# Optimization experiments

Measured on AMD Instinct MI355X. Metric: run time of the kernel, lower is better.

## Reference

```python
import jax, jax.numpy as jnp
import numpy as np

B, T, D, FF, H, K = 8, 1024, 512, 2048, 8, 15
HD = D // H  # key_dim = d_model // num_heads


def _ln(x, g, b):
    # keras LayerNormalization default epsilon = 1e-3
    m = jnp.mean(x, axis=-1, keepdims=True)
    v = jnp.var(x, axis=-1, keepdims=True)
    return (x - m) * jax.lax.rsqrt(v + 1e-3) * g + b


def setup_inputs() -> dict:
    key = jax.random.key(0)
    ks = iter(jax.random.split(key, 64))

    def rn(shape, s=0.02):
        return jax.random.normal(next(ks), shape, jnp.float32) * s

    p = {}
    p['x'] = jax.random.normal(next(ks), (B, T, D), jnp.float32)
    # ff_pre: LN -> Dense(FF, relu) -> Dense(D)
    p['g1'] = jnp.ones((D,), jnp.float32); p['b1'] = jnp.zeros((D,), jnp.float32)
    p['Wff1'] = rn((D, FF)); p['bff1'] = jnp.zeros((FF,), jnp.float32)
    p['Wff2'] = rn((FF, D)); p['bff2'] = jnp.zeros((D,), jnp.float32)
    # attention norm + MHA projections (keras EinsumDense shapes)
    p['ga'] = jnp.ones((D,), jnp.float32); p['ba'] = jnp.zeros((D,), jnp.float32)
    p['Wq'] = rn((D, H, HD)); p['bq'] = jnp.zeros((H, HD), jnp.float32)
    p['Wk'] = rn((D, H, HD)); p['bk'] = jnp.zeros((H, HD), jnp.float32)
    p['Wv'] = rn((D, H, HD)); p['bv'] = jnp.zeros((H, HD), jnp.float32)
    p['Wo'] = rn((H, HD, D)); p['bo'] = jnp.zeros((D,), jnp.float32)
    # conv branch: LN -> pointwise conv (2D, gelu) -> depthwise conv(k=15) -> BN -> swish -> pointwise conv (D)
    p['gc'] = jnp.ones((D,), jnp.float32); p['bc'] = jnp.zeros((D,), jnp.float32)
    p['Wcp'] = rn((D, 2 * D)); p['bcp'] = jnp.zeros((2 * D,), jnp.float32)
    p['dwk'] = rn((K, 1, 2 * D)); p['dwb'] = jnp.zeros((2 * D,), jnp.float32)
    p['bn_g'] = jnp.ones((2 * D,), jnp.float32); p['bn_b'] = jnp.zeros((2 * D,), jnp.float32)
    p['bn_m'] = jnp.zeros((2 * D,), jnp.float32)
    p['bn_v'] = jnp.ones((2 * D,), jnp.float32)
    p['Wco'] = rn((2 * D, D)); p['bco'] = jnp.zeros((D,), jnp.float32)
    # ff_post
    p['g2'] = jnp.ones((D,), jnp.float32); p['b2'] = jnp.zeros((D,), jnp.float32)
    p['Wf1'] = rn((D, FF)); p['bf1'] = jnp.zeros((FF,), jnp.float32)
    p['Wf2'] = rn((FF, D)); p['bf2'] = jnp.zeros((D,), jnp.float32)
    return p


def reference(x, g1, b1, Wff1, bff1, Wff2, bff2, ga, ba, Wq, bq, Wk, bk, Wv, bv, Wo, bo, gc, bc, Wcp, bcp, dwk, dwb, bn_g, bn_b, bn_m, bn_v, Wco, bco, g2, b2, Wf1, bf1, Wf2, bf2):
    # Macaron FFN (pre), half-step residual applied later
    x_ff = jnp.maximum(_ln(x, g1, b1) @ Wff1 + bff1, 0.0) @ Wff2 + bff2

    # causal multi-head self-attention (cache=None path)
    a = _ln(x, ga, ba)
    q = jnp.einsum('btd,dhk->bthk', a, Wq) + bq
    k = jnp.einsum('btd,dhk->bthk', a, Wk) + bk
    v = jnp.einsum('btd,dhk->bthk', a, Wv) + bv
    scores = jnp.einsum('bqhd,bkhd->bhqk', q, k) / jnp.sqrt(jnp.float32(HD))
    causal = jnp.tril(jnp.ones((T, T), bool))  # [T,T]
    scores = jnp.where(causal, scores, jnp.float32(-1e9))
    w = jax.nn.softmax(scores, axis=-1)
    ctx = jnp.einsum('bhqk,bkhd->bqhd', w, v)
    attn = jnp.einsum('bqhd,hdo->bqo', ctx, Wo) + bo

    x = x + 0.5 * x_ff + attn

    # convolution module: pointwise(gelu) -> causal left-pad -> depthwise -> BN(inference) -> swish -> pointwise
    c = jax.nn.gelu(_ln(x, gc, bc) @ Wcp + bcp, approximate=False)
    c = jnp.pad(c, ((0, 0), (K - 1, 0), (0, 0)))  # causal pad
    c = jax.lax.conv_general_dilated(
        c, dwk, window_strides=(1,), padding='VALID',
        dimension_numbers=('NWC', 'WIO', 'NWC'), feature_group_count=2 * D) + dwb
    c = (c - bn_m) * jax.lax.rsqrt(bn_v + 1e-3) * bn_g + bn_b
    c = c * jax.nn.sigmoid(c)  # swish
    c = c @ Wco + bco
    x = x + c

    # post FFN (full residual)
    x = x + (jnp.maximum(_ln(x, g2, b2) @ Wf1 + bf1, 0.0) @ Wf2 + bf2)
    return x
```

## Files before the change

kernel.cpp:

```cpp
#include <hip/hip_runtime.h>
#include <hip/hip_bf16.h>
#include <math.h>

#define BB 8
#define TT 1024
#define DD 512
#define FFD 2048
#define HH 8
#define HDD 64
#define KW 15
#define MR (BB*TT)
#define QKVN 1536

typedef __attribute__((ext_vector_type(8))) short short8;
typedef __attribute__((ext_vector_type(4))) short short4v;
typedef __attribute__((ext_vector_type(4))) float f32x4;
typedef __hip_bfloat16 bf16;

__device__ __forceinline__ float bf2f(unsigned u16) {
    return __uint_as_float(u16 << 16);
}

__device__ __forceinline__ void async_copy16(const void* g, void* l) {
    __builtin_amdgcn_global_load_lds(
        (const __attribute__((address_space(1))) void*)g,
        (__attribute__((address_space(3))) void*)l, 16, 0, 0);
}

__device__ __forceinline__ float gelu_exact(float v) {
    return 0.5f * v * (1.0f + erff(v * 0.70710678118654752f));
}

struct PrepPack {
    const float* src[10];
    bf16*        dst[10];
    int          K[10];
    int          lgNT[10];
    float        scale[10];
    int          off[10];
    const float* bq; const float* bk; const float* bv;
    float*       bdst;
    const float* x;
    const float* g1; const float* b1; const float* ga; const float* ba;
    bf16* o1; bf16* o2;
};

__global__ __launch_bounds__(256) void prep_kernel(PrepPack P) {
    __shared__ alignas(16) bf16 T[64][72];
    const int bid = blockIdx.x;
    if (bid == 1536) {
        #pragma unroll
        for (int it = 0; it < 6; ++it) {
            int i = it * 256 + threadIdx.x;
            float v = i < 512 ? P.bq[i] * 0.125f
                              : (i < 1024 ? P.bk[i - 512] : P.bv[i - 1024]);
            P.bdst[i] = v;
        }
        return;
    }
    if (bid > 1536) {
        int wave = ((bid - 1537) * 256 + (int)threadIdx.x) >> 6;
        int lane = threadIdx.x & 63;
        const float* row = P.x + (size_t)wave * DD;
        float4 v0 = ((const float4*)row)[lane];
        float4 v1 = ((const float4*)row)[64 + lane];
        float s  = v0.x + v0.y + v0.z + v0.w + v1.x + v1.y + v1.z + v1.w;
        float ss = v0.x*v0.x + v0.y*v0.y + v0.z*v0.z + v0.w*v0.w
                 + v1.x*v1.x + v1.y*v1.y + v1.z*v1.z + v1.w*v1.w;
        #pragma unroll
        for (int off = 32; off >= 1; off >>= 1) {
            s  += __shfl_xor(s,  off, 64);
            ss += __shfl_xor(ss, off, 64);
        }
        float mean = s * (1.0f / DD);
        float var  = ss * (1.0f / DD) - mean * mean;
        float r    = rsqrtf(var + 1e-3f);
        float n0x = (v0.x - mean) * r, n0y = (v0.y - mean) * r,
              n0z = (v0.z - mean) * r, n0w = (v0.w - mean) * r;
        float n1x = (v1.x - mean) * r, n1y = (v1.y - mean) * r,
              n1z = (v1.z - mean) * r, n1w = (v1.w - mean) * r;
        {
            float4 g0 = ((const float4*)P.g1)[lane];
            float4 gg = ((const float4*)P.g1)[64 + lane];
            float4 b0 = ((const float4*)P.b1)[lane];
            float4 bb = ((const float4*)P.b1)[64 + lane];
            alignas(8) bf16 o0[4], o1[4];
            o0[0] = __float2bfloat16(n0x * g0.x + b0.x);
            o0[1] = __float2bfloat16(n0y * g0.y + b0.y);
            o0[2] = __float2bfloat16(n0z * g0.z + b0.z);
            o0[3] = __float2bfloat16(n0w * g0.w + b0.w);
            o1[0] = __float2bfloat16(n1x * gg.x + bb.x);
            o1[1] = __float2bfloat16(n1y * gg.y + bb.y);
            o1[2] = __float2bfloat16(n1z * gg.z + bb.z);
            o1[3] = __float2bfloat16(n1w * gg.w + bb.w);
            bf16* orow = P.o1 + (size_t)wave * DD;
            *(short4v*)(orow + lane * 4)       = *(const short4v*)o0;
            *(short4v*)(orow + 256 + lane * 4) = *(const short4v*)o1;
        }
        {
            float4 g0 = ((const float4*)P.ga)[lane];
            float4 gg = ((const float4*)P.ga)[64 + lane];
            float4 b0 = ((const float4*)P.ba)[lane];
            float4 bb = ((const float4*)P.ba)[64 + lane];
            alignas(8) bf16 o0[4], o1[4];
            o0[0] = __float2bfloat16(n0x * g0.x + b0.x);
            o0[1] = __float2bfloat16(n0y * g0.y + b0.y);
            o0[2] = __float2bfloat16(n0z * g0.z + b0.z);
            o0[3] = __float2bfloat16(n0w * g0.w + b0.w);
            o1[0] = __float2bfloat16(n1x * gg.x + bb.x);
            o1[1] = __float2bfloat16(n1y * gg.y + bb.y);
            o1[2] = __float2bfloat16(n1z * gg.z + bb.z);
            o1[3] = __float2bfloat16(n1w * gg.w + bb.w);
            bf16* orow = P.o2 + (size_t)wave * DD;
            *(short4v*)(orow + lane * 4)       = *(const short4v*)o0;
            *(short4v*)(orow + 256 + lane * 4) = *(const short4v*)o1;
        }
        return;
    }
    int e = 0;
    #pragma unroll
    for (int i = 1; i < 10; ++i) e = (bid >= P.off[i]) ? i : e;
    const float* W  = P.src[e];
    bf16*        Wt = P.dst[e];
    const int    K  = P.K[e];
    const int    lg = P.lgNT[e];
    const float  scale = P.scale[e];
    const int local = bid - P.off[e];
    const int bx = local & ((1 << lg) - 1);
    const int by = local >> lg;
    const int k0 = by * 64;
    const int n0 = bx * 64;
    const int N  = (1 << lg) * 64;
    const int tid = threadIdx.x;
    #pragma unroll
    for (int it = 0; it < 4; ++it) {
        int lin = it * 256 + tid;
        int kl  = lin >> 4;
        int nq  = (lin & 15) * 4;
        float4 v = *(const float4*)(W + (size_t)(k0 + kl) * N + n0 + nq);
        T[nq + 0][kl] = __float2bfloat16(v.x * scale);
        T[nq + 1][kl] = __float2bfloat16(v.y * scale);
        T[nq + 2][kl] = __float2bfloat16(v.z * scale);
        T[nq + 3][kl] = __float2bfloat16(v.w * scale);
    }
    __syncthreads();
    #pragma unroll
    for (int it = 0; it < 4; ++it) {
        int lin = it * 256 + tid;
        int nl  = lin >> 4;
        int kq  = (lin & 15) * 4;
        *(short4v*)(Wt + (size_t)(n0 + nl) * K + k0 + kq) = *(const short4v*)&T[nl][kq];
    }
}

__global__ __launch_bounds__(256) void ln_kernel(const float* __restrict__ x,
                                                 const float* __restrict__ g,
                                                 const float* __restrict__ b,
                                                 bf16* __restrict__ out) {
    int wave = (blockIdx.x * blockDim.x + threadIdx.x) >> 6;
    int lane = threadIdx.x & 63;
    if (wave >= MR) return;
    const float* row = x + (size_t)wave * DD;
    float4 v0 = ((const float4*)row)[lane];
    float4 v1 = ((const float4*)row)[64 + lane];
    float s  = v0.x + v0.y + v0.z + v0.w + v1.x + v1.y + v1.z + v1.w;
    float ss = v0.x*v0.x + v0.y*v0.y + v0.z*v0.z + v0.w*v0.w
             + v1.x*v1.x + v1.y*v1.y + v1.z*v1.z + v1.w*v1.w;
    #pragma unroll
    for (int off = 32; off >= 1; off >>= 1) {
        s  += __shfl_xor(s,  off, 64);
        ss += __shfl_xor(ss, off, 64);
    }
    float mean = s * (1.0f / DD);
    float var  = ss * (1.0f / DD) - mean * mean;
    float r    = rsqrtf(var + 1e-3f);
    float4 g0 = ((const float4*)g)[lane];
    float4 g1 = ((const float4*)g)[64 + lane];
    float4 b0 = ((const float4*)b)[lane];
    float4 b1 = ((const float4*)b)[64 + lane];
    alignas(8) bf16 o0[4], o1[4];
    o0[0] = __float2bfloat16((v0.x - mean) * r * g0.x + b0.x);
    o0[1] = __float2bfloat16((v0.y - mean) * r * g0.y + b0.y);
    o0[2] = __float2bfloat16((v0.z - mean) * r * g0.z + b0.z);
    o0[3] = __float2bfloat16((v0.w - mean) * r * g0.w + b0.w);
    o1[0] = __float2bfloat16((v1.x - mean) * r * g1.x + b1.x);
    o1[1] = __float2bfloat16((v1.y - mean) * r * g1.y + b1.y);
    o1[2] = __float2bfloat16((v1.z - mean) * r * g1.z + b1.z);
    o1[3] = __float2bfloat16((v1.w - mean) * r * g1.w + b1.w);
    bf16* orow = out + (size_t)wave * DD;
    *(short4v*)(orow + lane * 4)       = *(const short4v*)o0;
    *(short4v*)(orow + 256 + lane * 4) = *(const short4v*)o1;
}

template<int BN, int OP, int RESMODE, int OUTMODE>
__global__ __launch_bounds__(256) void bgemm_kernel(
    const bf16* __restrict__ A,
    const bf16* __restrict__ Bt,
    const float* __restrict__ bias,
    const float* __restrict__ res1,
    const bf16* __restrict__ res2,
    float s2, float oscale,
    void* __restrict__ Cout,
    int N, int Kd, int nxb)
{
    constexpr int NT = BN / 32;
    __shared__ alignas(16) bf16 As[128][64];
    __shared__ alignas(16) bf16 Bs[BN][64];
    const int tid  = threadIdx.x;
    const int w    = tid >> 6;
    const int lane = tid & 63;
    const int quad = lane >> 4;
    const int l16  = lane & 15;
    const int wm   = w >> 1, wn = w & 1;

    const int flat = blockIdx.x;
    const int c8   = flat & 7;
    const int j    = flat >> 3;
    const int jy   = j / nxb;
    const int m0   = (c8 * 8 + jy) * 128;
    const int n0   = (j - jy * nxb) * BN;

    const int srow = lane >> 3;
    const int scol = ((lane & 7) ^ srow) * 8;

    const bf16* Ap = A  + (size_t)(m0 + w * 32 + srow) * Kd + scol;
    const bf16* Bp = Bt + (size_t)(n0 + w * (BN / 4) + srow) * Kd + scol;

    f32x4 acc[4][NT] = {};

    for (int k0 = 0; k0 < Kd; k0 += 64) {
        #pragma unroll
        for (int i = 0; i < 4; ++i)
            async_copy16(Ap + (size_t)(i * 8) * Kd + k0, &As[w * 32 + i * 8][0]);
        #pragma unroll
        for (int i = 0; i < BN / 32; ++i)
            async_copy16(Bp + (size_t)(i * 8) * Kd + k0, &Bs[w * (BN / 4) + i * 8][0]);
        __syncthreads();
        #pragma unroll
        for (int ks = 0; ks < 2; ++ks) {
            short8 af[4], bfr[NT];
            #pragma unroll
            for (int mt = 0; mt < 4; ++mt) {
                const int row = wm * 64 + mt * 16 + l16;
                const int c   = ((ks * 4 + quad) ^ (row & 7)) * 16;
                af[mt] = *(const short8*)((const char*)&As[row][0] + c);
            }
            #pragma unroll
            for (int nt = 0; nt < NT; ++nt) {
                const int col = wn * (BN / 2) + nt * 16 + l16;
                const int c   = ((ks * 4 + quad) ^ (col & 7)) * 16;
                bfr[nt] = *(const short8*)((const char*)&Bs[col][0] + c);
            }
            #pragma unroll
            for (int mt = 0; mt < 4; ++mt)
                #pragma unroll
                for (int nt = 0; nt < NT; ++nt)
                    acc[mt][nt] = __builtin_amdgcn_mfma_f32_16x16x32_bf16(
                        af[mt], bfr[nt], acc[mt][nt], 0, 0, 0);
        }
        __syncthreads();
    }

    const int crow0 = m0 + wm * 64 + quad * 4;
    const int ccol0 = n0 + wn * (BN / 2) + l16;
    #pragma unroll
    for (int nt = 0; nt < NT; ++nt) {
        const int col = ccol0 + nt * 16;
        const float bv = bias[col];
        #pragma unroll
        for (int mt = 0; mt < 4; ++mt) {
            #pragma unroll
            for (int r = 0; r < 4; ++r) {
                const int row = crow0 + mt * 16 + r;
                const size_t off = (size_t)row * N + col;
                float o = acc[mt][nt][r] + bv;
                if (OP == 1)      o = fmaxf(o, 0.f);
                else if (OP == 2) o = gelu_exact(o);
                if (RESMODE >= 1) o += res1[off];
                if (RESMODE == 2) o += s2 * __bfloat162float(res2[off]);
                if (OUTMODE == 0) ((float*)Cout)[off] = o;
                else              ((bf16*)Cout)[off]  = __float2bfloat16(o * oscale);
            }
        }
    }
}

__global__ __launch_bounds__(256) void ffqkv_kernel(
    const bf16* __restrict__ lnb, const bf16* __restrict__ lnab,
    const bf16* __restrict__ Wff1t, const bf16* __restrict__ Wqkvt,
    const float* __restrict__ bff1, const float* __restrict__ bqkv,
    bf16* __restrict__ bigb, bf16* __restrict__ qkvb, bf16* __restrict__ Vtb)
{
    __shared__ alignas(16) bf16 As[128][64];
    __shared__ alignas(16) bf16 Bs[128][64];
    const int tid  = threadIdx.x;
    const int w    = tid >> 6;
    const int lane = tid & 63;
    const int quad = lane >> 4;
    const int l16  = lane & 15;
    const int wm   = w >> 1, wn = w & 1;

    const bool jobq = blockIdx.x >= 1024;
    const int  flat = jobq ? (int)blockIdx.x - 1024 : (int)blockIdx.x;
    const int  nxb  = jobq ? 12 : 16;
    const int  N    = jobq ? QKVN : FFD;
    const bf16* A   = jobq ? lnab : lnb;
    const bf16* Bt  = jobq ? Wqkvt : Wff1t;
    const float* bias = jobq ? bqkv : bff1;

    const int c8 = flat & 7;
    const int j  = flat >> 3;
    const int jy = j / nxb;
    const int m0 = (c8 * 8 + jy) * 128;
    const int n0 = (j - jy * nxb) * 128;

    const int srow = lane >> 3;
    const int scol = ((lane & 7) ^ srow) * 8;

    const bf16* Ap = A  + (size_t)(m0 + w * 32 + srow) * DD + scol;
    const bf16* Bp = Bt + (size_t)(n0 + w * 32 + srow) * DD + scol;

    f32x4 acc[4][4] = {};

    for (int k0 = 0; k0 < DD; k0 += 64) {
        #pragma unroll
        for (int i = 0; i < 4; ++i) {
            async_copy16(Ap + (size_t)(i * 8) * DD + k0, &As[w * 32 + i * 8][0]);
            async_copy16(Bp + (size_t)(i * 8) * DD + k0, &Bs[w * 32 + i * 8][0]);
        }
        __syncthreads();
        #pragma unroll
        for (int ks = 0; ks < 2; ++ks) {
            short8 af[4], bfr[4];
            #pragma unroll
            for (int mt = 0; mt < 4; ++mt) {
                const int row = wm * 64 + mt * 16 + l16;
                const int c   = ((ks * 4 + quad) ^ (row & 7)) * 16;
                af[mt] = *(const short8*)((const char*)&As[row][0] + c);
            }
            #pragma unroll
            for (int nt = 0; nt < 4; ++nt) {
                const int col = wn * 64 + nt * 16 + l16;
                const int c   = ((ks * 4 + quad) ^ (col & 7)) * 16;
                bfr[nt] = *(const short8*)((const char*)&Bs[col][0] + c);
            }
            #pragma unroll
            for (int mt = 0; mt < 4; ++mt)
                #pragma unroll
                for (int nt = 0; nt < 4; ++nt)
                    acc[mt][nt] = __builtin_amdgcn_mfma_f32_16x16x32_bf16(
                        af[mt], bfr[nt], acc[mt][nt], 0, 0, 0);
        }
        __syncthreads();
    }

    const int crow0 = m0 + wm * 64 + quad * 4;
    const int ccol0 = n0 + wn * 64 + l16;
    #pragma unroll
    for (int nt = 0; nt < 4; ++nt) {
        const int col = ccol0 + nt * 16;
        const float bv = bias[col];
        #pragma unroll
        for (int mt = 0; mt < 4; ++mt) {
            if (jobq) {
                alignas(8) bf16 o4[4];
                #pragma unroll
                for (int r = 0; r < 4; ++r)
                    o4[r] = __float2bfloat16(acc[mt][nt][r] + bv);
                if (col < 1024) {
                    #pragma unroll
                    for (int r = 0; r < 4; ++r)
                        qkvb[(size_t)(crow0 + mt * 16 + r) * QKVN + col] = o4[r];
                } else {
                    const int dg   = col - 1024;
                    const int rowt = crow0 + mt * 16;
                    const int bb   = rowt >> 10, t0 = rowt & 1023;
                    const int bh2  = bb * 8 + (dg >> 6), d = dg & 63;
                    *(short4v*)(Vtb + ((size_t)bh2 * 64 + d) * TT + t0) =
                        *(const short4v*)o4;
                }
            } else {
                #pragma unroll
                for (int r = 0; r < 4; ++r) {
                    const float o = fmaxf(acc[mt][nt][r] + bv, 0.f);
                    bigb[(size_t)(crow0 + mt * 16 + r) * FFD + col] =
                        __float2bfloat16(o);
                }
            }
        }
    }
}

__global__ __launch_bounds__(256) void ff2attn_kernel(
    const bf16* __restrict__ QKV, const bf16* __restrict__ Vt,
    bf16* __restrict__ ctx,
    const bf16* __restrict__ bigb, const bf16* __restrict__ Wff2t,
    const float* __restrict__ bff2, bf16* __restrict__ xffb)
{
    __shared__ alignas(16) bf16 smem[16384];
    const int tid  = threadIdx.x;
    const int w    = tid >> 6;
    const int lane = tid & 63;
    const int quad = lane >> 4;
    const int l16  = lane & 15;

    if (blockIdx.x < 512) {
        typedef bf16 (*tile_t)[64][64];
        tile_t Ks = (tile_t)smem;
        tile_t Vs = (tile_t)(smem + 2 * 64 * 64);
        const int bh = blockIdx.x & 63;
        const int bi = 7 - ((int)blockIdx.x >> 6);
        const int b = bh >> 3, h = bh & 7;

        const bf16* Qg = QKV + (size_t)(b * TT) * QKVN + h * 64;
        const bf16* Kg = QKV + (size_t)(b * TT) * QKVN + 512 + h * 64;
        const bf16* Vg = Vt  + (size_t)bh * 64 * TT;

        const int qL = bi * 128 + w * 16;
        const int qH = qL + 64;
        short8 qfL0 = *(const short8*)(Qg + (size_t)(qL + l16) * QKVN + quad * 8);
        short8 qfL1 = *(const short8*)(Qg + (size_t)(qL + l16) * QKVN + 32 + quad * 8);
        short8 qfH0 = *(const short8*)(Qg + (size_t)(qH + l16) * QKVN + quad * 8);
        short8 qfH1 = *(const short8*)(Qg + (size_t)(qH + l16) * QKVN + 32 + quad * 8);

        const int sgrow  = lane >> 3;
        const int sgchnk = lane & 7;

        f32x4 caccL[4] = {}, caccH[4] = {};
        float lL = 0.f, lH = 0.f;
        const int prow_base = ((l16 >> 2) << 3) + (l16 & 3);
        const int smax = 2 * bi + 1;

        #pragma unroll
        for (int i = 0; i < 2; ++i) {
            const int rowbase = w * 8 + i * 32;
            const int row = rowbase + sgrow;
            const int fR = (row & 3) | (((row >> 3) & 1) << 2);
            const int sc = sgchnk ^ fR;
            async_copy16(Kg + (size_t)row * QKVN + sc * 8, &Ks[0][rowbase][0]);
            async_copy16(Vg + (size_t)row * TT + sc * 8,   &Vs[0][rowbase][0]);
        }

        int buf = 0;
        for (int s = 0; s <= smax; ++s) {
            __syncthreads();
            if (s < smax) {
                const int kn = (s + 1) * 64;
                #pragma unroll
                for (int i = 0; i < 2; ++i) {
                    const int rowbase = w * 8 + i * 32;
                    const int row = rowbase + sgrow;
                    const int fR = (row & 3) | (((row >> 3) & 1) << 2);
                    const int sc = sgchnk ^ fR;
                    async_copy16(Kg + (size_t)(kn + row) * QKVN + sc * 8,
                                 &Ks[buf ^ 1][rowbase][0]);
                    async_copy16(Vg + (size_t)row * TT + kn + sc * 8,
                                 &Vs[buf ^ 1][rowbase][0]);
                }
            }
            const int k0 = s * 64;
            const bool doL = (s < smax);

            f32x4 sTL[4], sTH[4];
            #pragma unroll
            for (int s4 = 0; s4 < 4; ++s4) {
                const int prow = prow_base + (s4 >> 1) * 32 + (s4 & 1) * 4;
                const int fR = (prow & 3) | (((prow >> 3) & 1) << 2);
                short8 ka = *(const short8*)&Ks[buf][prow][(quad ^ fR) * 8];
                short8 kb = *(const short8*)&Ks[buf][prow][((4 + quad) ^ fR) * 8];
                f32x4 zH = {0.f, 0.f, 0.f, 0.f};
                zH = __builtin_amdgcn_mfma_f32_16x16x32_bf16(ka, qfH0, zH, 0, 0, 0);
                sTH[s4] = __builtin_amdgcn_mfma_f32_16x16x32_bf16(kb, qfH1, zH, 0, 0, 0);
                if (doL) {
                    f32x4 zL = {0.f, 0.f, 0.f, 0.f};
                    zL = __builtin_amdgcn_mfma_f32_16x16x32_bf16(ka, qfL0, zL, 0, 0, 0);
                    sTL[s4] = __builtin_amdgcn_mfma_f32_16x16x32_bf16(kb, qfL1, zL, 0, 0, 0);
                }
            }

            alignas(16) bf16 pbH[16], pbL[16];
            if (s == smax) {
                const int qg = qH + l16;
                #pragma unroll
                for (int s4 = 0; s4 < 4; ++s4)
                    #pragma unroll
                    for (int r = 0; r < 4; ++r) {
                        const int key = k0 + (s4 >> 1) * 32 + quad * 8 + (s4 & 1) * 4 + r;
                        const float p = (key <= qg) ? __expf(sTH[s4][r]) : 0.f;
                        lH += p;
                        pbH[s4 * 4 + r] = __float2bfloat16(p);
                    }
            } else {
                #pragma unroll
                for (int s4 = 0; s4 < 4; ++s4)
                    #pragma unroll
                    for (int r = 0; r < 4; ++r) {
                        const float p = __expf(sTH[s4][r]);
                        lH += p;
                        pbH[s4 * 4 + r] = __float2bfloat16(p);
                    }
            }
            if (doL) {
                if (s == smax - 1) {
                    const int qg = qL + l16;
                    #pragma unroll
                    for (int s4 = 0; s4 < 4; ++s4)
                        #pragma unroll
                        for (int r = 0; r < 4; ++r) {
                            const int key = k0 + (s4 >> 1) * 32 + quad * 8 + (s4 & 1) * 4 + r;
                            const float p = (key <= qg) ? __expf(sTL[s4][r]) : 0.f;
                            lL += p;
                            pbL[s4 * 4 + r] = __float2bfloat16(p);
                        }
                } else {
                    #pragma unroll
                    for (int s4 = 0; s4 < 4; ++s4)
                        #pragma unroll
                        for (int r = 0; r < 4; ++r) {
                            const float p = __expf(sTL[s4][r]);
                            lL += p;
                            pbL[s4 * 4 + r] = __float2bfloat16(p);
                        }
                }
            }
            const short8 pfH0 = *(const short8*)&pbH[0];
            const short8 pfH1 = *(const short8*)&pbH[8];
            const short8 pfL0 = *(const short8*)&pbL[0];
            const short8 pfL1 = *(const short8*)&pbL[8];

            #pragma unroll
            for (int g = 0; g < 4; ++g) {
                const int vrow = g * 16 + l16;
                const int fR = (vrow & 3) | (((vrow >> 3) & 1) << 2);
                short8 va = *(const short8*)&Vs[buf][vrow][(quad ^ fR) * 8];
                short8 vb = *(const short8*)&Vs[buf][vrow][((4 + quad) ^ fR) * 8];
                caccH[g] = __builtin_amdgcn_mfma_f32_16x16x32_bf16(va, pfH0, caccH[g], 0, 0, 0);
                caccH[g] = __builtin_amdgcn_mfma_f32_16x16x32_bf16(vb, pfH1, caccH[g], 0, 0, 0);
                if (doL) {
                    caccL[g] = __builtin_amdgcn_mfma_f32_16x16x32_bf16(va, pfL0, caccL[g], 0, 0, 0);
                    caccL[g] = __builtin_amdgcn_mfma_f32_16x16x32_bf16(vb, pfL1, caccL[g], 0, 0, 0);
                }
            }
            buf ^= 1;
        }

        lL += __shfl_xor(lL, 16, 64);
        lL += __shfl_xor(lL, 32, 64);
        lH += __shfl_xor(lH, 16, 64);
        lH += __shfl_xor(lH, 32, 64);
        const float invL = 1.0f / lL;
        const float invH = 1.0f / lH;

        bf16* CbL = ctx + (size_t)(b * TT + qL + l16) * DD + h * 64;
        bf16* CbH = ctx + (size_t)(b * TT + qH + l16) * DD + h * 64;
        #pragma unroll
        for (int g = 0; g < 4; ++g) {
            alignas(8) bf16 oL[4], oH[4];
            #pragma unroll
            for (int r = 0; r < 4; ++r) {
                oL[r] = __float2bfloat16(caccL[g][r] * invL);
                oH[r] = __float2bfloat16(caccH[g][r] * invH);
            }
            *(short4v*)(CbL + g * 16 + quad * 4) = *(const short4v*)oL;
            *(short4v*)(CbH + g * 16 + quad * 4) = *(const short4v*)oH;
        }
    } else {
        typedef bf16 (*row_t)[64];
        row_t As = (row_t)smem;
        row_t Bs = (row_t)(smem + 128 * 64);
        const int wm = w >> 1, wn = w & 1;

        const int flat = (int)blockIdx.x - 512;
        const int c8 = flat & 7;
        const int j  = flat >> 3;
        const int jy = j >> 3;
        const int m0 = (c8 * 8 + jy) * 128;
        const int n0 = (j & 7) * 64;

        const int srow = lane >> 3;
        const int scol = ((lane & 7) ^ srow) * 8;

        const bf16* Ap = bigb  + (size_t)(m0 + w * 32 + srow) * FFD + scol;
        const bf16* Bp = Wff2t + (size_t)(n0 + w * 16 + srow) * FFD + scol;

        f32x4 acc[4][2] = {};

        for (int k0 = 0; k0 < FFD; k0 += 64) {
            #pragma unroll
            for (int i = 0; i < 4; ++i)
                async_copy16(Ap + (size_t)(i * 8) * FFD + k0, &As[w * 32 + i * 8][0]);
            #pragma unroll
            for (int i = 0; i < 2; ++i)
                async_copy16(Bp + (size_t)(i * 8) * FFD + k0, &Bs[w * 16 + i * 8][0]);
            __syncthreads();
            #pragma unroll
            for (int ks = 0; ks < 2; ++ks) {
                short8 af[4], bfr[2];
                #pragma unroll
                for (int mt = 0; mt < 4; ++mt) {
                    const int row = wm * 64 + mt * 16 + l16;
                    const int c   = ((ks * 4 + quad) ^ (row & 7)) * 16;
                    af[mt] = *(const short8*)((const char*)&As[row][0] + c);
                }
                #pragma unroll
                for (int nt = 0; nt < 2; ++nt) {
                    const int col = wn * 32 + nt * 16 + l16;
                    const int c   = ((ks * 4 + quad) ^ (col & 7)) * 16;
                    bfr[nt] = *(const short8*)((const char*)&Bs[col][0] + c);
                }
                #pragma unroll
                for (int mt = 0; mt < 4; ++mt)
                    #pragma unroll
                    for (int nt = 0; nt < 2; ++nt)
                        acc[mt][nt] = __builtin_amdgcn_mfma_f32_16x16x32_bf16(
                            af[mt], bfr[nt], acc[mt][nt], 0, 0, 0);
            }
            __syncthreads();
        }

        const int crow0 = m0 + wm * 64 + quad * 4;
        const int ccol0 = n0 + wn * 32 + l16;
        #pragma unroll
        for (int nt = 0; nt < 2; ++nt) {
            const int col = ccol0 + nt * 16;
            const float bv = bff2[col];
            #pragma unroll
            for (int mt = 0; mt < 4; ++mt)
                #pragma unroll
                for (int r = 0; r < 4; ++r) {
                    const int row = crow0 + mt * 16 + r;
                    xffb[(size_t)row * DD + col] =
                        __float2bfloat16(acc[mt][nt][r] + bv);
                }
        }
    }
}

__global__ __launch_bounds__(256) void dwconv_kernel(const bf16* __restrict__ c1,
                                                     const float* __restrict__ dwk,
                                                     const float* __restrict__ dwb,
                                                     const float* __restrict__ bn_g,
                                                     const float* __restrict__ bn_b,
                                                     const float* __restrict__ bn_m,
                                                     const float* __restrict__ bn_v,
                                                     bf16* __restrict__ out) {
    const int C2 = 2 * DD;
    const int lin = blockIdx.x * 256 + threadIdx.x;
    const int chp = lin & 511;
    const int ch  = chp << 1;
    const int tch = lin >> 9;
    const int row0 = tch << 4;
    const int t0   = row0 & (TT - 1);

    float w0[KW], w1[KW];
    #pragma unroll
    for (int i = 0; i < KW; ++i) {
        w0[i] = dwk[i * C2 + ch];
        w1[i] = dwk[i * C2 + ch + 1];
    }
    const float a0 = rsqrtf(bn_v[ch] + 1e-3f) * bn_g[ch];
    const float a1 = rsqrtf(bn_v[ch + 1] + 1e-3f) * bn_g[ch + 1];
    const float c0 = (dwb[ch] - bn_m[ch]) * a0 + bn_b[ch];
    const float c1v = (dwb[ch + 1] - bn_m[ch + 1]) * a1 + bn_b[ch + 1];

    float x0[30], x1[30];
    if (t0 >= KW - 1) {
        #pragma unroll
        for (int i = 0; i < 30; ++i) {
            unsigned u = *(const unsigned*)(c1 + (size_t)(row0 - (KW - 1) + i) * C2 + ch);
            x0[i] = bf2f(u & 0xffff);
            x1[i] = bf2f(u >> 16);
        }
    } else {
        #pragma unroll
        for (int i = 0; i < 30; ++i) {
            unsigned u = 0;
            if (t0 - (KW - 1) + i >= 0)
                u = *(const unsigned*)(c1 + (size_t)(row0 - (KW - 1) + i) * C2 + ch);
            x0[i] = bf2f(u & 0xffff);
            x1[i] = bf2f(u >> 16);
        }
    }

    #pragma unroll
    for (int j = 0; j < 16; ++j) {
        float s0 = 0.f, s1 = 0.f;
        #pragma unroll
        for (int i = 0; i < KW; ++i) {
            s0 += x0[j + i] * w0[i];
            s1 += x1[j + i] * w1[i];
        }
        s0 = s0 * a0 + c0;
        s1 = s1 * a1 + c1v;
        s0 = s0 / (1.f + __expf(-s0));
        s1 = s1 / (1.f + __expf(-s1));
        alignas(4) bf16 ob[2] = {__float2bfloat16(s0), __float2bfloat16(s1)};
        *(unsigned*)(out + (size_t)(row0 + j) * C2 + ch) = *(const unsigned*)ob;
    }
}

extern "C" void kernel_launch(void* const* d_in, const int* in_sizes, int n_in,
                              void* d_out, int out_size, void* d_ws, size_t ws_size,
                              hipStream_t stream) {
    const float* x    = (const float*)d_in[0];
    const float* g1   = (const float*)d_in[1];
    const float* b1   = (const float*)d_in[2];
    const float* Wff1 = (const float*)d_in[3];
    const float* bff1 = (const float*)d_in[4];
    const float* Wff2 = (const float*)d_in[5];
    const float* bff2 = (const float*)d_in[6];
    const float* ga   = (const float*)d_in[7];
    const float* ba   = (const float*)d_in[8];
    const float* Wq   = (const float*)d_in[9];
    const float* bq   = (const float*)d_in[10];
    const float* Wk   = (const float*)d_in[11];
    const float* bk   = (const float*)d_in[12];
    const float* Wv   = (const float*)d_in[13];
    const float* bv   = (const float*)d_in[14];
    const float* Wo   = (const float*)d_in[15];
    const float* bo   = (const float*)d_in[16];
    const float* gc   = (const float*)d_in[17];
    const float* bc   = (const float*)d_in[18];
    const float* Wcp  = (const float*)d_in[19];
    const float* bcp  = (const float*)d_in[20];
    const float* dwk  = (const float*)d_in[21];
    const float* dwb  = (const float*)d_in[22];
    const float* bn_g = (const float*)d_in[23];
    const float* bn_b = (const float*)d_in[24];
    const float* bn_m = (const float*)d_in[25];
    const float* bn_v = (const float*)d_in[26];
    const float* Wco  = (const float*)d_in[27];
    const float* bco  = (const float*)d_in[28];
    const float* g2   = (const float*)d_in[29];
    const float* b2   = (const float*)d_in[30];
    const float* Wf1  = (const float*)d_in[31];
    const float* bf1  = (const float*)d_in[32];
    const float* Wf2  = (const float*)d_in[33];
    const float* bf2  = (const float*)d_in[34];

    float* out = (float*)d_out;

    char* p = (char*)d_ws;
    bf16* lnb   = (bf16*)p;  p += (size_t)MR * DD * 2;
    bf16* lnab  = (bf16*)p;  p += (size_t)MR * DD * 2;
    bf16* qkvb  = (bf16*)p;  p += (size_t)MR * QKVN * 2;
    bf16* Vtb   = (bf16*)p;  p += (size_t)MR * DD * 2;
    bf16* ctxb  = (bf16*)p;  p += (size_t)MR * DD * 2;
    bf16* xffb  = (bf16*)p;  p += (size_t)MR * DD * 2;
    bf16* bigb  = (bf16*)p;  p += (size_t)MR * FFD * 2;
    bf16* c2b   = (bf16*)p;  p += (size_t)MR * 1024 * 2;
    bf16* Wff1t = (bf16*)p;  p += (size_t)FFD * DD * 2;
    bf16* Wff2t = (bf16*)p;  p += (size_t)DD * FFD * 2;
    bf16* Wqkvt = (bf16*)p;  p += (size_t)QKVN * DD * 2;
    bf16* Wot   = (bf16*)p;  p += (size_t)DD * DD * 2;
    bf16* Wcpt  = (bf16*)p;  p += (size_t)1024 * DD * 2;
    bf16* Wcot  = (bf16*)p;  p += (size_t)DD * 1024 * 2;
    bf16* Wf1t  = (bf16*)p;  p += (size_t)FFD * DD * 2;
    bf16* Wf2t  = (bf16*)p;  p += (size_t)DD * FFD * 2;
    float* bqkv = (float*)p; p += QKVN * 4;

    dim3 blk(256);

    PrepPack P;
    auto set = [&](int i, const float* s, bf16* d, int K, int N, float sc, int off) {
        P.src[i] = s; P.dst[i] = d; P.K[i] = K; P.scale[i] = sc; P.off[i] = off;
        int nt = N / 64, lg = 0; while ((1 << lg) < nt) ++lg; P.lgNT[i] = lg;
    };
    set(0, Wff1, Wff1t, DD,  FFD, 1.f,    0);
    set(1, Wff2, Wff2t, FFD, DD,  1.f,    256);
    set(2, Wq,   Wqkvt,                DD, DD, 0.125f, 512);
    set(3, Wk,   Wqkvt + (size_t)512 * DD,  DD, DD, 1.f, 576);
    set(4, Wv,   Wqkvt + (size_t)1024 * DD, DD, DD, 1.f, 640);
    set(5, Wo,   Wot,   DD,  DD,  1.f,    704);
    set(6, Wcp,  Wcpt,  DD,  1024, 1.f,   768);
    set(7, Wco,  Wcot,  1024, DD, 1.f,    896);
    set(8, Wf1,  Wf1t,  DD,  FFD, 1.f,    1024);
    set(9, Wf2,  Wf2t,  FFD, DD,  1.f,    1280);
    P.bq = bq; P.bk = bk; P.bv = bv; P.bdst = bqkv;
    P.x = x; P.g1 = g1; P.b1 = b1; P.ga = ga; P.ba = ba;
    P.o1 = lnb; P.o2 = lnab;

    prep_kernel<<<dim3(1537 + MR / 4), blk, 0, stream>>>(P);
    ffqkv_kernel<<<dim3(1024 + 768), blk, 0, stream>>>(
        lnb, lnab, Wff1t, Wqkvt, bff1, bqkv, bigb, qkvb, Vtb);
    ff2attn_kernel<<<dim3(1024), blk, 0, stream>>>(
        qkvb, Vtb, ctxb, bigb, Wff2t, bff2, xffb);
    bgemm_kernel<64, 0, 2, 0><<<dim3(8 * 64), blk, 0, stream>>>(
        ctxb, Wot, bo, x, xffb, 0.5f, 1.f, out, DD, DD, 8);
    ln_kernel<<<dim3(MR / 4), blk, 0, stream>>>(out, gc, bc, lnb);
    bgemm_kernel<128, 2, 0, 1><<<dim3(8 * 64), blk, 0, stream>>>(
        lnb, Wcpt, bcp, nullptr, nullptr, 0.f, 1.f, bigb, 1024, DD, 8);
    dwconv_kernel<<<dim3(MR * 512 / 16 / 256), blk, 0, stream>>>(
        bigb, dwk, dwb, bn_g, bn_b, bn_m, bn_v, c2b);
    bgemm_kernel<64, 0, 1, 0><<<dim3(8 * 64), blk, 0, stream>>>(
        c2b, Wcot, bco, out, nullptr, 0.f, 1.f, out, DD, 1024, 8);
    ln_kernel<<<dim3(MR / 4), blk, 0, stream>>>(out, g2, b2, lnb);
    bgemm_kernel<128, 1, 0, 1><<<dim3(16 * 64), blk, 0, stream>>>(
        lnb, Wf1t, bf1, nullptr, nullptr, 0.f, 1.f, bigb, FFD, DD, 16);
    bgemm_kernel<64, 0, 1, 0><<<dim3(8 * 64), blk, 0, stream>>>(
        bigb, Wf2t, bf2, out, nullptr, 0.f, 1.f, out, DD, FFD, 8);
}
```

Before: 381.8 us.

## Replace 128x128 FF1/QKV GEMMs with double-buffered 256x256 tile kernel

Replaces the 128x128-tile fused FF1+QKV GEMM kernel with a 256x256-tile, 512-thread kernel. It double-buffers 64-wide K chunks in 128KB of LDS and interleaves async global-to-LDS copies with MFMA clusters, using explicit barriers, waitcnts and setprio. The same kernel also replaces the post-FFN first GEMM. The aim is more operand reuse per tile and overlap of loads with compute, at the cost of fewer blocks (448 and 256), so less parallelism and a risk of tail imbalance on a large-CU GPU. The hand-written waitcnt and barrier schedule is fragile.

```diff
diff --git a/kernel.cpp b/kernel.cpp
--- a/kernel.cpp
+++ b/kernel.cpp
@@ -285,105 +285,151 @@
     }
 }
 
-__global__ __launch_bounds__(256) void ffqkv_kernel(
-    const bf16* __restrict__ lnb, const bf16* __restrict__ lnab,
-    const bf16* __restrict__ Wff1t, const bf16* __restrict__ Wqkvt,
-    const float* __restrict__ bff1, const float* __restrict__ bqkv,
-    bf16* __restrict__ bigb, bf16* __restrict__ qkvb, bf16* __restrict__ Vtb)
+__global__ __launch_bounds__(512, 2) void gemm256_kernel(
+    const bf16* __restrict__ Aff, const bf16* __restrict__ Btff,
+    const float* __restrict__ biasff, bf16* __restrict__ outff,
+    const bf16* __restrict__ Aqk, const bf16* __restrict__ Btqk,
+    const float* __restrict__ biasqk, bf16* __restrict__ qkvb,
+    bf16* __restrict__ Vtb, int nffblk)
 {
-    __shared__ alignas(16) bf16 As[128][64];
-    __shared__ alignas(16) bf16 Bs[128][64];
+    __shared__ alignas(16) char lds[131072];
     const int tid  = threadIdx.x;
     const int w    = tid >> 6;
     const int lane = tid & 63;
     const int quad = lane >> 4;
     const int l16  = lane & 15;
-    const int wm   = w >> 1, wn = w & 1;
-
-    const bool jobq = blockIdx.x >= 1024;
-    const int  flat = jobq ? (int)blockIdx.x - 1024 : (int)blockIdx.x;
-    const int  nxb  = jobq ? 12 : 16;
-    const int  N    = jobq ? QKVN : FFD;
-    const bf16* A   = jobq ? lnab : lnb;
-    const bf16* Bt  = jobq ? Wqkvt : Wff1t;
-    const float* bias = jobq ? bqkv : bff1;
+    const int wm   = w >> 2, wn = w & 3;
+
+    const bool jobq = (int)blockIdx.x >= nffblk;
+    const int  flat = jobq ? (int)blockIdx.x - nffblk : (int)blockIdx.x;
+    const int  nxb  = jobq ? 6 : 8;
+    const bf16* A   = jobq ? Aqk : Aff;
+    const bf16* Bt  = jobq ? Btqk : Btff;
+    const float* bias = jobq ? biasqk : biasff;
 
     const int c8 = flat & 7;
     const int j  = flat >> 3;
     const int jy = j / nxb;
-    const int m0 = (c8 * 8 + jy) * 128;
-    const int n0 = (j - jy * nxb) * 128;
-
-    const int srow = lane >> 3;
-    const int scol = ((lane & 7) ^ srow) * 8;
-
-    const bf16* Ap = A  + (size_t)(m0 + w * 32 + srow) * DD + scol;
-    const bf16* Bp = Bt + (size_t)(n0 + w * 32 + srow) * DD + scol;
-
-    f32x4 acc[4][4] = {};
-
-    for (int k0 = 0; k0 < DD; k0 += 64) {
-        #pragma unroll
-        for (int i = 0; i < 4; ++i) {
-            async_copy16(Ap + (size_t)(i * 8) * DD + k0, &As[w * 32 + i * 8][0]);
-            async_copy16(Bp + (size_t)(i * 8) * DD + k0, &Bs[w * 32 + i * 8][0]);
-        }
-        __syncthreads();
-        #pragma unroll
-        for (int ks = 0; ks < 2; ++ks) {
-            short8 af[4], bfr[4];
-            #pragma unroll
-            for (int mt = 0; mt < 4; ++mt) {
-                const int row = wm * 64 + mt * 16 + l16;
-                const int c   = ((ks * 4 + quad) ^ (row & 7)) * 16;
-                af[mt] = *(const short8*)((const char*)&As[row][0] + c);
-            }
-            #pragma unroll
-            for (int nt = 0; nt < 4; ++nt) {
-                const int col = wn * 64 + nt * 16 + l16;
-                const int c   = ((ks * 4 + quad) ^ (col & 7)) * 16;
-                bfr[nt] = *(const short8*)((const char*)&Bs[col][0] + c);
-            }
-            #pragma unroll
-            for (int mt = 0; mt < 4; ++mt)
-                #pragma unroll
-                for (int nt = 0; nt < 4; ++nt)
-                    acc[mt][nt] = __builtin_amdgcn_mfma_f32_16x16x32_bf16(
-                        af[mt], bfr[nt], acc[mt][nt], 0, 0, 0);
-        }
-        __syncthreads();
-    }
-
-    const int crow0 = m0 + wm * 64 + quad * 4;
+    const int m0 = (c8 * 4 + jy) * 256;
+    const int n0 = (j - jy * nxb) * 256;
+
+    const bf16* ApS = A  + (size_t)(m0 + w * 32 + (lane >> 2)) * DD + (lane & 3) * 8;
+    const bf16* BpS = Bt + (size_t)(n0 + w * 32 + (lane >> 2)) * DD + (lane & 3) * 8;
+    char* ldsW = lds + w * 2048;
+
+#define STAGE_A(kc, boff) do { \
+        async_copy16(ApS + (kc),            ldsW + (boff));        \
+        async_copy16(ApS + 16 * DD + (kc),  ldsW + (boff) + 1024); } while (0)
+#define STAGE_B(kc, boff) do { \
+        async_copy16(BpS + (kc),            ldsW + (boff));        \
+        async_copy16(BpS + 16 * DD + (kc),  ldsW + (boff) + 1024); } while (0)
+
+    const int aoff = (wm * 128 + l16) * 64 + quad * 16;
+    const int boff = 32768 + (wn * 64 + l16) * 64 + quad * 16;
+
+    f32x4 acc[8][4] = {};
+
+#define CLUSTER(MH) \
+    asm volatile("" ::: "memory"); \
+    __builtin_amdgcn_s_barrier(); \
+    asm volatile("s_waitcnt lgkmcnt(0)" ::: "memory"); \
+    __builtin_amdgcn_sched_barrier(0); \
+    __builtin_amdgcn_s_setprio(1); \
+    _Pragma("unroll") \
+    for (int mt = 0; mt < 4; ++mt) \
+        _Pragma("unroll") \
+        for (int nt = 0; nt < 4; ++nt) \
+            acc[(MH) * 4 + mt][nt] = __builtin_amdgcn_mfma_f32_16x16x32_bf16( \
+                af[mt], bf[nt], acc[(MH) * 4 + mt][nt], 0, 0, 0); \
+    __builtin_amdgcn_s_setprio(0); \
+    asm volatile("" ::: "memory"); \
+    __builtin_amdgcn_s_barrier();
+
+    STAGE_A(0,  0);      STAGE_B(0,  32768);
+    STAGE_A(32, 16384);  STAGE_B(32, 49152);
+    STAGE_A(64, 65536);  STAGE_B(64, 65536 + 32768);
+    asm volatile("s_waitcnt vmcnt(4)" ::: "memory");
+    __builtin_amdgcn_s_barrier();
+
+    for (int t = 0; t < 8; ++t) {
+        const int cb = (t & 1) * 65536;
+        const int nb = cb ^ 65536;
+        short8 af[4], bf[4];
+
+        #pragma unroll
+        for (int nt = 0; nt < 4; ++nt)
+            bf[nt] = *(const short8*)(lds + cb + boff + nt * 1024);
+        #pragma unroll
+        for (int mt = 0; mt < 4; ++mt)
+            af[mt] = *(const short8*)(lds + cb + aoff + mt * 1024);
+        if (t < 7) STAGE_A((t + 1) * 64 + 32, nb + 16384);
+        CLUSTER(0)
+
+        #pragma unroll
+        for (int mt = 0; mt < 4; ++mt)
+            af[mt] = *(const short8*)(lds + cb + aoff + 4096 + mt * 1024);
+        if (t < 7) STAGE_B((t + 1) * 64 + 32, nb + 49152);
+        CLUSTER(1)
+
+        #pragma unroll
+        for (int nt = 0; nt < 4; ++nt)
+            bf[nt] = *(const short8*)(lds + cb + 16384 + boff + nt * 1024);
+        #pragma unroll
+        for (int mt = 0; mt < 4; ++mt)
+            af[mt] = *(const short8*)(lds + cb + 16384 + aoff + mt * 1024);
+        if (t < 6) STAGE_A((t + 2) * 64, cb);
+        CLUSTER(0)
+
+        #pragma unroll
+        for (int mt = 0; mt < 4; ++mt)
+            af[mt] = *(const short8*)(lds + cb + 16384 + aoff + 4096 + mt * 1024);
+        if (t < 6) STAGE_B((t + 2) * 64, cb + 32768);
+        if (t < 6)       { asm volatile("s_waitcnt vmcnt(4)" ::: "memory"); }
+        else if (t == 6) { asm volatile("s_waitcnt vmcnt(0)" ::: "memory"); }
+        CLUSTER(1)
+    }
+#undef CLUSTER
+#undef STAGE_A
+#undef STAGE_B
+
+    const int crow0 = m0 + wm * 128 + quad * 4;
     const int ccol0 = n0 + wn * 64 + l16;
-    #pragma unroll
-    for (int nt = 0; nt < 4; ++nt) {
-        const int col = ccol0 + nt * 16;
-        const float bv = bias[col];
-        #pragma unroll
-        for (int mt = 0; mt < 4; ++mt) {
-            if (jobq) {
+    if (jobq) {
+        #pragma unroll
+        for (int nt = 0; nt < 4; ++nt) {
+            const int col = ccol0 + nt * 16;
+            const float bv = bias[col];
+            #pragma unroll
+            for (int mt = 0; mt < 8; ++mt) {
                 alignas(8) bf16 o4[4];
                 #pragma unroll
                 for (int r = 0; r < 4; ++r)
                     o4[r] = __float2bfloat16(acc[mt][nt][r] + bv);
+                const int rowt = crow0 + mt * 16;
                 if (col < 1024) {
                     #pragma unroll
                     for (int r = 0; r < 4; ++r)
-                        qkvb[(size_t)(crow0 + mt * 16 + r) * QKVN + col] = o4[r];
+                        qkvb[(size_t)(rowt + r) * QKVN + col] = o4[r];
                 } else {
-                    const int dg   = col - 1024;
-                    const int rowt = crow0 + mt * 16;
-                    const int bb   = rowt >> 10, t0 = rowt & 1023;
-                    const int bh2  = bb * 8 + (dg >> 6), d = dg & 63;
+                    const int dg  = col - 1024;
+                    const int bb  = rowt >> 10, t0 = rowt & 1023;
+                    const int bh2 = bb * 8 + (dg >> 6), d = dg & 63;
                     *(short4v*)(Vtb + ((size_t)bh2 * 64 + d) * TT + t0) =
                         *(const short4v*)o4;
                 }
-            } else {
+            }
+        }
+    } else {
+        #pragma unroll
+        for (int nt = 0; nt < 4; ++nt) {
+            const int col = ccol0 + nt * 16;
+            const float bv = bias[col];
+            #pragma unroll
+            for (int mt = 0; mt < 8; ++mt) {
                 #pragma unroll
                 for (int r = 0; r < 4; ++r) {
                     const float o = fmaxf(acc[mt][nt][r] + bv, 0.f);
-                    bigb[(size_t)(crow0 + mt * 16 + r) * FFD + col] =
+                    outff[(size_t)(crow0 + mt * 16 + r) * FFD + col] =
                         __float2bfloat16(o);
                 }
             }
@@ -781,8 +827,8 @@
     P.o1 = lnb; P.o2 = lnab;
 
     prep_kernel<<<dim3(1537 + MR / 4), blk, 0, stream>>>(P);
-    ffqkv_kernel<<<dim3(1024 + 768), blk, 0, stream>>>(
-        lnb, lnab, Wff1t, Wqkvt, bff1, bqkv, bigb, qkvb, Vtb);
+    gemm256_kernel<<<dim3(448), dim3(512), 0, stream>>>(
+        lnb, Wff1t, bff1, bigb, lnab, Wqkvt, bqkv, qkvb, Vtb, 256);
     ff2attn_kernel<<<dim3(1024), blk, 0, stream>>>(
         qkvb, Vtb, ctxb, bigb, Wff2t, bff2, xffb);
     bgemm_kernel<64, 0, 2, 0><<<dim3(8 * 64), blk, 0, stream>>>(
@@ -795,8 +841,8 @@
     bgemm_kernel<64, 0, 1, 0><<<dim3(8 * 64), blk, 0, stream>>>(
         c2b, Wcot, bco, out, nullptr, 0.f, 1.f, out, DD, 1024, 8);
     ln_kernel<<<dim3(MR / 4), blk, 0, stream>>>(out, g2, b2, lnb);
-    bgemm_kernel<128, 1, 0, 1><<<dim3(16 * 64), blk, 0, stream>>>(
-        lnb, Wf1t, bf1, nullptr, nullptr, 0.f, 1.f, bigb, FFD, DD, 16);
+    gemm256_kernel<<<dim3(256), dim3(512), 0, stream>>>(
+        lnb, Wf1t, bf1, bigb, nullptr, nullptr, nullptr, nullptr, nullptr, 256);
     bgemm_kernel<64, 0, 1, 0><<<dim3(8 * 64), blk, 0, stream>>>(
         bigb, Wf2t, bf2, out, nullptr, 0.f, 1.f, out, DD, FFD, 8);
 }
```

Result: no change. 374.7 us (-1.9%).
